# Performance work log

Measured on AMD Instinct MI355X. Metric: run time of the kernel, lower is better.

The kernel has to match this reference:

```python
import jax, jax.numpy as jnp
import numpy as np

BATCH = 8192
NUM_STOCKS = 4096


def setup_inputs() -> dict:
    key = jax.random.key(0)
    f = jax.random.normal(key, (BATCH, NUM_STOCKS), dtype=jnp.float32)
    return {"f": f, "num_stocks": NUM_STOCKS}


def reference(f, num_stocks):
    # Original torch loop computes, for each i, logsumexp(f[:, i:]) — i.e. all
    # suffix logsumexps. That is exactly a reverse cumulative logsumexp along
    # the stock axis, done here in a single O(n) fused scan instead of O(n^2).
    suffix_lse = jax.lax.cumlogsumexp(f, axis=1, reverse=True)  # [B, N]
    l = -jnp.sum(f, axis=1) + jnp.sum(suffix_lse, axis=1)       # [B]
    return jnp.mean(l)
```

## Files before the change

kernel.cpp:

```cpp
#include <hip/hip_runtime.h>
#include <math.h>

#define BATCH 8192
#define NSTK  4096
#define TPB   256
#define EPT   16

#define LN2f    (0.6931471805599453f)
#define LOG2Ef  (1.4426950408889634f)

__device__ __forceinline__ float fexp2(float x) { return __builtin_amdgcn_exp2f(x); }
__device__ __forceinline__ float flog2(float x) { return __builtin_amdgcn_logf(x); }

#define SBUF_WORDS (4096 + 256)

__global__ __launch_bounds__(TPB) void suffix_lse_rows(const float* __restrict__ f,
                                                       float* __restrict__ row_out) {
    __shared__ float sbuf[SBUF_WORDS];
    __shared__ float wsum_s[4], wsum_p[4];

    const int row  = blockIdx.x;
    const int tid  = threadIdx.x;
    const int lane = tid & 63;
    const int wave = tid >> 6;

    const float4* p4 = reinterpret_cast<const float4*>(f + (size_t)row * NSTK);

    float sumg = 0.f;
#pragma unroll
    for (int k = 0; k < 4; ++k) {
        int gidx = (k << 8) + tid;
        float4 v = p4[gidx];
        float gx = v.x * LOG2Ef, gy = v.y * LOG2Ef,
              gz = v.z * LOG2Ef, gw = v.w * LOG2Ef;
        sumg += (gx + gy) + (gz + gw);
        int w = (gidx << 2) + ((gidx >> 4) << 2);
        *reinterpret_cast<float4*>(&sbuf[w]) =
            make_float4(fexp2(gx), fexp2(gy), fexp2(gz), fexp2(gw));
    }
    __syncthreads();

    float e[EPT];
#pragma unroll
    for (int i = 0; i < 4; ++i) {
        int idx = (tid << 4) + (i << 2);
        int w = idx + ((idx >> 6) << 2);
        float4 v = *reinterpret_cast<const float4*>(&sbuf[w]);
        e[4 * i + 0] = v.x;
        e[4 * i + 1] = v.y;
        e[4 * i + 2] = v.z;
        e[4 * i + 3] = v.w;
    }

    float cs = 0.f;
#pragma unroll
    for (int j = 0; j < EPT; ++j) cs += e[j];

    float is = cs;
#pragma unroll
    for (int d = 1; d < 64; d <<= 1) {
        float os = __shfl_down(is, d);
        if (lane + d < 64) is += os;
    }
    float es = __shfl_down(is, 1);
    if (lane == 63) es = 0.f;

    if (lane == 0) wsum_s[wave] = is;
    __syncthreads();
    float R = es;
#pragma unroll
    for (int w = 0; w < 4; ++w)
        if (w > wave) R += wsum_s[w];

    float S = R;
    float acc = 0.f;
#pragma unroll
    for (int j = EPT - 1; j >= 0; --j) {
        S += e[j];
        acc += flog2(S);
    }
    float part = acc - sumg;

#pragma unroll
    for (int d = 32; d > 0; d >>= 1) part += __shfl_down(part, d);
    if (lane == 0) wsum_p[wave] = part;
    __syncthreads();
    if (tid == 0)
        row_out[row] = LN2f * (wsum_p[0] + wsum_p[1] + wsum_p[2] + wsum_p[3]);
}

__global__ __launch_bounds__(1024) void reduce_mean(const float* __restrict__ row_vals,
                                                    float* __restrict__ out) {
    const int tid  = threadIdx.x;
    const int lane = tid & 63;
    const int wave = tid >> 6;
    double acc = 0.0;
#pragma unroll
    for (int i = 0; i < BATCH / 1024; ++i) acc += (double)row_vals[tid + i * 1024];
#pragma unroll
    for (int d = 32; d > 0; d >>= 1) acc += __shfl_down(acc, d);
    __shared__ double ws[16];
    if (lane == 0) ws[wave] = acc;
    __syncthreads();
    if (wave == 0) {
        double t = (lane < 16) ? ws[lane] : 0.0;
#pragma unroll
        for (int d = 8; d > 0; d >>= 1) t += __shfl_down(t, d);
        if (lane == 0) out[0] = (float)(t / (double)BATCH);
    }
}

extern "C" void kernel_launch(void* const* d_in, const int* in_sizes, int n_in,
                              void* d_out, int out_size, void* d_ws, size_t ws_size,
                              hipStream_t stream) {
    const float* f   = (const float*)d_in[0];
    float*       row = (float*)d_ws;
    float*       out = (float*)d_out;
    suffix_lse_rows<<<BATCH, TPB, 0, stream>>>(f, row);
    reduce_mean<<<1, 1024, 0, stream>>>(row, out);
}
```

Before: 28.02 us.

## Drop LDS transpose, scan per float4 group in registers, merge logs via products

Each thread now keeps its four coalesced float4 loads in registers instead of staging exponentials through shared memory and re-reading them as contiguous 16-element chunks. The suffix sum is built from four separate wave-level scans, one per column group, combined through a small shared array of per-wave group totals. The sixteen per-element log2 calls are replaced by running products of four suffix sums per group, followed by two log2 calls on paired products. This removes the LDS round trip and most transcendental work, at the cost of four times as many wave shuffles. The products of eight suffix sums also carry some fp32 overflow and precision risk.

```diff
diff --git a/kernel.cpp b/kernel.cpp
--- a/kernel.cpp
+++ b/kernel.cpp
@@ -4,7 +4,6 @@
 #define BATCH 8192
 #define NSTK  4096
 #define TPB   256
-#define EPT   16
 
 #define LN2f    (0.6931471805599453f)
 #define LOG2Ef  (1.4426950408889634f)
@@ -12,81 +11,91 @@
 __device__ __forceinline__ float fexp2(float x) { return __builtin_amdgcn_exp2f(x); }
 __device__ __forceinline__ float flog2(float x) { return __builtin_amdgcn_logf(x); }
 
-#define SBUF_WORDS (4096 + 256)
-
 __global__ __launch_bounds__(TPB) void suffix_lse_rows(const float* __restrict__ f,
                                                        float* __restrict__ row_out) {
-    __shared__ float sbuf[SBUF_WORDS];
-    __shared__ float wsum_s[4], wsum_p[4];
+    __shared__ float wag[4][4];
+    __shared__ float wsum_p[4];
 
-    const int row  = blockIdx.x;
     const int tid  = threadIdx.x;
     const int lane = tid & 63;
     const int wave = tid >> 6;
 
-    const float4* p4 = reinterpret_cast<const float4*>(f + (size_t)row * NSTK);
+    const float4* p4 = reinterpret_cast<const float4*>(f + (size_t)blockIdx.x * NSTK);
 
+    float4 v0 = p4[tid];
+    float4 v1 = p4[256 + tid];
+    float4 v2 = p4[512 + tid];
+    float4 v3 = p4[768 + tid];
+
+    float e[4][4];
+    float es[4];
     float sumg = 0.f;
-#pragma unroll
-    for (int k = 0; k < 4; ++k) {
-        int gidx = (k << 8) + tid;
-        float4 v = p4[gidx];
-        float gx = v.x * LOG2Ef, gy = v.y * LOG2Ef,
-              gz = v.z * LOG2Ef, gw = v.w * LOG2Ef;
-        sumg += (gx + gy) + (gz + gw);
-        int w = (gidx << 2) + ((gidx >> 4) << 2);
-        *reinterpret_cast<float4*>(&sbuf[w]) =
-            make_float4(fexp2(gx), fexp2(gy), fexp2(gz), fexp2(gw));
+
+#define GROUP_STAGE(k, vk)                                              \
+    {                                                                   \
+        float gx = vk.x * LOG2Ef, gy = vk.y * LOG2Ef,                   \
+              gz = vk.z * LOG2Ef, gw = vk.w * LOG2Ef;                   \
+        sumg += (gx + gy) + (gz + gw);                                  \
+        e[k][0] = fexp2(gx); e[k][1] = fexp2(gy);                       \
+        e[k][2] = fexp2(gz); e[k][3] = fexp2(gw);                       \
+        float is = (e[k][0] + e[k][1]) + (e[k][2] + e[k][3]);           \
+        _Pragma("unroll")                                               \
+        for (int d = 1; d < 64; d <<= 1) {                              \
+            float os = __shfl_down(is, d);                              \
+            if (lane + d < 64) is += os;                                \
+        }                                                               \
+        float ex = __shfl_down(is, 1);                                  \
+        if (lane == 63) ex = 0.f;                                       \
+        es[k] = ex;                                                     \
+        if (lane == 0) wag[k][wave] = is;   \
     }
+
+    GROUP_STAGE(0, v0)
+    GROUP_STAGE(1, v1)
+    GROUP_STAGE(2, v2)
+    GROUP_STAGE(3, v3)
+#undef GROUP_STAGE
+
     __syncthreads();
 
-    float e[EPT];
-#pragma unroll
-    for (int i = 0; i < 4; ++i) {
-        int idx = (tid << 4) + (i << 2);
-        int w = idx + ((idx >> 6) << 2);
-        float4 v = *reinterpret_cast<const float4*>(&sbuf[w]);
-        e[4 * i + 0] = v.x;
-        e[4 * i + 1] = v.y;
-        e[4 * i + 2] = v.z;
-        e[4 * i + 3] = v.w;
+    const float4* wagv = reinterpret_cast<const float4*>(&wag[0][0]);
+    float4 a0 = wagv[0], a1 = wagv[1], a2 = wagv[2], a3 = wagv[3];
+
+#define CROSS(a) ((wave < 1 ? (a).y : 0.f) + (wave < 2 ? (a).z : 0.f) + (wave < 3 ? (a).w : 0.f))
+    float c0 = CROSS(a0), c1 = CROSS(a1), c2 = CROSS(a2), c3 = CROSS(a3);
+#undef CROSS
+    float G1 = (a1.x + a1.y) + (a1.z + a1.w);
+    float G2 = (a2.x + a2.y) + (a2.z + a2.w);
+    float G3 = (a3.x + a3.y) + (a3.z + a3.w);
+    float SG2 = G3;
+    float SG1 = G3 + G2;
+    float SG0 = SG1 + G1;
+
+    float P0, P1, P2, P3;
+#define GROUP_SWEEP(k, Pk, SGk, ck)                                     \
+    {                                                                   \
+        float S = es[k] + ck + SGk;                                     \
+        S += e[k][3]; float P = S;                                      \
+        S += e[k][2]; P *= S;                                           \
+        S += e[k][1]; P *= S;                                           \
+        S += e[k][0]; P *= S;                                           \
+        Pk = P;                                                         \
     }
+    GROUP_SWEEP(3, P3, 0.f, c3)
+    GROUP_SWEEP(2, P2, SG2, c2)
+    GROUP_SWEEP(1, P1, SG1, c1)
+    GROUP_SWEEP(0, P0, SG0, c0)
+#undef GROUP_SWEEP
 
-    float cs = 0.f;
-#pragma unroll
-    for (int j = 0; j < EPT; ++j) cs += e[j];
-
-    float is = cs;
-#pragma unroll
-    for (int d = 1; d < 64; d <<= 1) {
-        float os = __shfl_down(is, d);
-        if (lane + d < 64) is += os;
-    }
-    float es = __shfl_down(is, 1);
-    if (lane == 63) es = 0.f;
-
-    if (lane == 0) wsum_s[wave] = is;
-    __syncthreads();
-    float R = es;
-#pragma unroll
-    for (int w = 0; w < 4; ++w)
-        if (w > wave) R += wsum_s[w];
-
-    float S = R;
-    float acc = 0.f;
-#pragma unroll
-    for (int j = EPT - 1; j >= 0; --j) {
-        S += e[j];
-        acc += flog2(S);
-    }
-    float part = acc - sumg;
+    float part = (flog2(P3 * P2) + flog2(P1 * P0)) - sumg;
 
 #pragma unroll
     for (int d = 32; d > 0; d >>= 1) part += __shfl_down(part, d);
     if (lane == 0) wsum_p[wave] = part;
     __syncthreads();
     if (tid == 0)
-        row_out[row] = LN2f * (wsum_p[0] + wsum_p[1] + wsum_p[2] + wsum_p[3]);
+        row_out[blockIdx.x] =
+            LN2f * ((wsum_p[0] + wsum_p[1]) + (wsum_p[2] + wsum_p[3]));
 }
 
 __global__ __launch_bounds__(1024) void reduce_mean(const float* __restrict__ row_vals,
```

Result: slower. 28.98 us (+3.4%).

## Fuse row reduction into main kernel via fixed-point atomics and last-block finish

Applied to the files above, without the earlier changes.

Removes the separate mean-reduction kernel. Each block instead atomically adds its row value, quantized to 64-bit fixed point, into one of 64 spread accumulators, and a two-level arrival counter lets the last block sum them and write the mean. A memset of the workspace is added to reset the counters. This trades one kernel launch for a memset plus per-block atomics, and the quantization changes precision slightly.

```diff
diff --git a/kernel.cpp b/kernel.cpp
--- a/kernel.cpp
+++ b/kernel.cpp
@@ -5,26 +5,32 @@
 #define NSTK  4096
 #define TPB   256
 #define EPT   16
+#define NBLK  BATCH
+#define NCOH  64
+#define BPC   (NBLK / NCOH)
 
 #define LN2f    (0.6931471805599453f)
 #define LOG2Ef  (1.4426950408889634f)
+#define QSCALE  65536.0
 
 __device__ __forceinline__ float fexp2(float x) { return __builtin_amdgcn_exp2f(x); }
 __device__ __forceinline__ float flog2(float x) { return __builtin_amdgcn_logf(x); }
 
 #define SBUF_WORDS (4096 + 256)
 
-__global__ __launch_bounds__(TPB) void suffix_lse_rows(const float* __restrict__ f,
-                                                       float* __restrict__ row_out) {
+__global__ __launch_bounds__(TPB) void suffix_lse_fused(const float* __restrict__ f,
+                                                        unsigned long long* __restrict__ acc,
+                                                        unsigned int* __restrict__ l1,
+                                                        unsigned int* __restrict__ l2,
+                                                        float* __restrict__ out) {
     __shared__ float sbuf[SBUF_WORDS];
     __shared__ float wsum_s[4], wsum_p[4];
 
-    const int row  = blockIdx.x;
     const int tid  = threadIdx.x;
     const int lane = tid & 63;
     const int wave = tid >> 6;
 
-    const float4* p4 = reinterpret_cast<const float4*>(f + (size_t)row * NSTK);
+    const float4* p4 = reinterpret_cast<const float4*>(f + (size_t)blockIdx.x * NSTK);
 
     float sumg = 0.f;
 #pragma unroll
@@ -73,49 +79,47 @@
         if (w > wave) R += wsum_s[w];
 
     float S = R;
-    float acc = 0.f;
+    float accL = 0.f;
 #pragma unroll
     for (int j = EPT - 1; j >= 0; --j) {
         S += e[j];
-        acc += flog2(S);
+        accL += flog2(S);
     }
-    float part = acc - sumg;
+    float part = accL - sumg;
 
 #pragma unroll
     for (int d = 32; d > 0; d >>= 1) part += __shfl_down(part, d);
     if (lane == 0) wsum_p[wave] = part;
     __syncthreads();
-    if (tid == 0)
-        row_out[row] = LN2f * (wsum_p[0] + wsum_p[1] + wsum_p[2] + wsum_p[3]);
-}
 
-__global__ __launch_bounds__(1024) void reduce_mean(const float* __restrict__ row_vals,
-                                                    float* __restrict__ out) {
-    const int tid  = threadIdx.x;
-    const int lane = tid & 63;
-    const int wave = tid >> 6;
-    double acc = 0.0;
+    if (tid == 0) {
+        float rowval = LN2f * ((wsum_p[0] + wsum_p[1]) + (wsum_p[2] + wsum_p[3]));
+        const int coh = blockIdx.x & (NCOH - 1);
+        long long q = llrint((double)rowval * QSCALE);
+        unsigned long long old = atomicAdd(&acc[coh], (unsigned long long)q);
+        asm volatile("" :: "v"(old));
+        unsigned o1 = atomicAdd(&l1[coh], 1u);
+        if (o1 == BPC - 1) {
+            unsigned o2 = atomicAdd(l2, 1u);
+            if (o2 == NCOH - 1) {
+                long long tot = 0;
 #pragma unroll
-    for (int i = 0; i < BATCH / 1024; ++i) acc += (double)row_vals[tid + i * 1024];
-#pragma unroll
-    for (int d = 32; d > 0; d >>= 1) acc += __shfl_down(acc, d);
-    __shared__ double ws[16];
-    if (lane == 0) ws[wave] = acc;
-    __syncthreads();
-    if (wave == 0) {
-        double t = (lane < 16) ? ws[lane] : 0.0;
-#pragma unroll
-        for (int d = 8; d > 0; d >>= 1) t += __shfl_down(t, d);
-        if (lane == 0) out[0] = (float)(t / (double)BATCH);
+                for (int i = 0; i < NCOH; ++i)
+                    tot += (long long)atomicAdd(&acc[i], 0ull);
+                out[0] = (float)((double)tot / (QSCALE * (double)BATCH));
+            }
+        }
     }
 }
 
 extern "C" void kernel_launch(void* const* d_in, const int* in_sizes, int n_in,
                               void* d_out, int out_size, void* d_ws, size_t ws_size,
                               hipStream_t stream) {
-    const float* f   = (const float*)d_in[0];
-    float*       row = (float*)d_ws;
-    float*       out = (float*)d_out;
-    suffix_lse_rows<<<BATCH, TPB, 0, stream>>>(f, row);
-    reduce_mean<<<1, 1024, 0, stream>>>(row, out);
+    const float*        f   = (const float*)d_in[0];
+    unsigned long long* acc = (unsigned long long*)d_ws;
+    unsigned int*       l1  = (unsigned int*)((char*)d_ws + 512);
+    unsigned int*       l2  = (unsigned int*)((char*)d_ws + 768);
+    float*              out = (float*)d_out;
+    hipMemsetAsync(d_ws, 0, 1024, stream);
+    suffix_lse_fused<<<NBLK, TPB, 0, stream>>>(f, acc, l1, l2, out);
 }
```

Measured after the change: 63.27 us. 126% more time.

## Process four rows per block with register prefetch of the next row

Applied to the files above, without the earlier changes.

Each block now handles four consecutive rows instead of one, and the grid shrinks accordingly. While the exponentials for the current row are written to shared memory, the next row's data is already being loaded into registers, so global load latency overlaps with the scan work. Global loads also switch to nontemporal loads, since the input is read only once. The cost is fewer blocks to spread across the GPU and less parallelism available to hide latency, on a kernel that is already close to memory-bandwidth bound.

```diff
diff --git a/kernel.cpp b/kernel.cpp
--- a/kernel.cpp
+++ b/kernel.cpp
@@ -5,9 +5,13 @@
 #define NSTK  4096
 #define TPB   256
 #define EPT   16
+#define ROWS_PER_BLOCK 4
+#define NBLOCKS (BATCH / ROWS_PER_BLOCK)
 
 #define LN2f    (0.6931471805599453f)
 #define LOG2Ef  (1.4426950408889634f)
+
+typedef float f32x4 __attribute__((ext_vector_type(4)));
 
 __device__ __forceinline__ float fexp2(float x) { return __builtin_amdgcn_exp2f(x); }
 __device__ __forceinline__ float flog2(float x) { return __builtin_amdgcn_logf(x); }
@@ -19,74 +23,90 @@
     __shared__ float sbuf[SBUF_WORDS];
     __shared__ float wsum_s[4], wsum_p[4];
 
-    const int row  = blockIdx.x;
     const int tid  = threadIdx.x;
     const int lane = tid & 63;
     const int wave = tid >> 6;
+    const int row0 = blockIdx.x * ROWS_PER_BLOCK;
 
-    const float4* p4 = reinterpret_cast<const float4*>(f + (size_t)row * NSTK);
-
-    float sumg = 0.f;
+    f32x4 pf[4];
+    {
+        const f32x4* p4 = reinterpret_cast<const f32x4*>(f + (size_t)row0 * NSTK);
 #pragma unroll
-    for (int k = 0; k < 4; ++k) {
-        int gidx = (k << 8) + tid;
-        float4 v = p4[gidx];
-        float gx = v.x * LOG2Ef, gy = v.y * LOG2Ef,
-              gz = v.z * LOG2Ef, gw = v.w * LOG2Ef;
-        sumg += (gx + gy) + (gz + gw);
-        int w = (gidx << 2) + ((gidx >> 4) << 2);
-        *reinterpret_cast<float4*>(&sbuf[w]) =
-            make_float4(fexp2(gx), fexp2(gy), fexp2(gz), fexp2(gw));
-    }
-    __syncthreads();
-
-    float e[EPT];
-#pragma unroll
-    for (int i = 0; i < 4; ++i) {
-        int idx = (tid << 4) + (i << 2);
-        int w = idx + ((idx >> 6) << 2);
-        float4 v = *reinterpret_cast<const float4*>(&sbuf[w]);
-        e[4 * i + 0] = v.x;
-        e[4 * i + 1] = v.y;
-        e[4 * i + 2] = v.z;
-        e[4 * i + 3] = v.w;
+        for (int k = 0; k < 4; ++k)
+            pf[k] = __builtin_nontemporal_load(&p4[(k << 8) + tid]);
     }
 
-    float cs = 0.f;
+    for (int r = 0; r < ROWS_PER_BLOCK; ++r) {
+        float sumg = 0.f;
 #pragma unroll
-    for (int j = 0; j < EPT; ++j) cs += e[j];
+        for (int k = 0; k < 4; ++k) {
+            int gidx = (k << 8) + tid;
+            f32x4 v = pf[k];
+            float gx = v.x * LOG2Ef, gy = v.y * LOG2Ef,
+                  gz = v.z * LOG2Ef, gw = v.w * LOG2Ef;
+            sumg += (gx + gy) + (gz + gw);
+            int w = (gidx << 2) + ((gidx >> 4) << 2);
+            f32x4 ev = { fexp2(gx), fexp2(gy), fexp2(gz), fexp2(gw) };
+            *reinterpret_cast<f32x4*>(&sbuf[w]) = ev;
+        }
+        if (r + 1 < ROWS_PER_BLOCK) {
+            const f32x4* p4 =
+                reinterpret_cast<const f32x4*>(f + (size_t)(row0 + r + 1) * NSTK);
+#pragma unroll
+            for (int k = 0; k < 4; ++k)
+                pf[k] = __builtin_nontemporal_load(&p4[(k << 8) + tid]);
+        }
+        __syncthreads();
 
-    float is = cs;
+        float e[EPT];
 #pragma unroll
-    for (int d = 1; d < 64; d <<= 1) {
-        float os = __shfl_down(is, d);
-        if (lane + d < 64) is += os;
-    }
-    float es = __shfl_down(is, 1);
-    if (lane == 63) es = 0.f;
+        for (int i = 0; i < 4; ++i) {
+            int idx = (tid << 4) + (i << 2);
+            int w = idx + ((idx >> 6) << 2);
+            f32x4 v = *reinterpret_cast<const f32x4*>(&sbuf[w]);
+            e[4 * i + 0] = v.x;
+            e[4 * i + 1] = v.y;
+            e[4 * i + 2] = v.z;
+            e[4 * i + 3] = v.w;
+        }
 
-    if (lane == 0) wsum_s[wave] = is;
-    __syncthreads();
-    float R = es;
+        float cs = 0.f;
 #pragma unroll
-    for (int w = 0; w < 4; ++w)
-        if (w > wave) R += wsum_s[w];
+        for (int j = 0; j < EPT; ++j) cs += e[j];
 
-    float S = R;
-    float acc = 0.f;
+        float is = cs;
 #pragma unroll
-    for (int j = EPT - 1; j >= 0; --j) {
-        S += e[j];
-        acc += flog2(S);
-    }
-    float part = acc - sumg;
+        for (int d = 1; d < 64; d <<= 1) {
+            float os = __shfl_down(is, d);
+            if (lane + d < 64) is += os;
+        }
+        float es = __shfl_down(is, 1);
+        if (lane == 63) es = 0.f;
+
+        if (lane == 0) wsum_s[wave] = is;
+        __syncthreads();
+        float R = es;
+#pragma unroll
+        for (int w = 0; w < 4; ++w)
+            if (w > wave) R += wsum_s[w];
+
+        float S = R;
+        float accL = 0.f;
+#pragma unroll
+        for (int j = EPT - 1; j >= 0; --j) {
+            S += e[j];
+            accL += flog2(S);
+        }
+        float part = accL - sumg;
 
 #pragma unroll
-    for (int d = 32; d > 0; d >>= 1) part += __shfl_down(part, d);
-    if (lane == 0) wsum_p[wave] = part;
-    __syncthreads();
-    if (tid == 0)
-        row_out[row] = LN2f * (wsum_p[0] + wsum_p[1] + wsum_p[2] + wsum_p[3]);
+        for (int d = 32; d > 0; d >>= 1) part += __shfl_down(part, d);
+        if (lane == 0) wsum_p[wave] = part;
+        __syncthreads();
+        if (tid == 0)
+            row_out[row0 + r] =
+                LN2f * ((wsum_p[0] + wsum_p[1]) + (wsum_p[2] + wsum_p[3]));
+    }
 }
 
 __global__ __launch_bounds__(1024) void reduce_mean(const float* __restrict__ row_vals,
@@ -116,6 +136,6 @@
     const float* f   = (const float*)d_in[0];
     float*       row = (float*)d_ws;
     float*       out = (float*)d_out;
-    suffix_lse_rows<<<BATCH, TPB, 0, stream>>>(f, row);
+    suffix_lse_rows<<<NBLOCKS, TPB, 0, stream>>>(f, row);
     reduce_mean<<<1, 1024, 0, stream>>>(row, out);
 }
```

New measurement: 28.79 us. 2.8% more time.
